# Kernel optimization log

Measured on AMD Instinct MI355X. Metric: run time of the kernel, lower is better.

## Reference

```python
import jax, jax.numpy as jnp
import numpy as np

NUM_CHUNKS = 8
HEAD_DIM = 128
PROJ = 1024       # projection_size (q)
KV_PROJ = 1024    # kv_projection_size
NEG_INF = -1e30


def _rotate_half(x):
    x1, x2 = jnp.split(x, 2, axis=-1)
    return jnp.concatenate((-x2, x1), axis=-1)


def _apply_rope(x, cos, sin):
    # x: [B, S, H, D]; cos/sin: [B, S, 1, rot_dim] with rot_dim == D here
    return x * cos + _rotate_half(x) * sin


def setup_inputs() -> dict:
    key = jax.random.key(0)
    k1, k2, k3 = jax.random.split(key, 3)
    S, B, H = 8192, 1, 1024
    layernorm_output = jax.random.normal(k1, (S, B, H), dtype=jnp.float32)
    # rotary tables, stored [S, 1, 1, rot_dim] (seq-first, like the torch module)
    inv_freq = 1.0 / (10000.0 ** (jnp.arange(0, HEAD_DIM, 2, dtype=jnp.float32) / HEAD_DIM))
    t = jnp.arange(S, dtype=jnp.float32)
    freqs = jnp.einsum('s,d->sd', t, inv_freq)
    emb = jnp.concatenate((freqs, freqs), axis=-1)  # [S, rot_dim]
    freqs_cos = jnp.cos(emb)[:, None, None, :]
    freqs_sin = jnp.sin(emb)[:, None, None, :]
    qkv_weight = jax.random.normal(k2, (PROJ + 2 * KV_PROJ, H), dtype=jnp.float32) * (H ** -0.5)
    qkv_bias = jax.random.normal(k3, (PROJ + 2 * KV_PROJ,), dtype=jnp.float32) * 0.02
    return {
        'layernorm_output': layernorm_output,
        'freqs_cos': freqs_cos,
        'freqs_sin': freqs_sin,
        'qkv_weight': qkv_weight,
        'qkv_bias': qkv_bias,
    }


def reference(layernorm_output, freqs_cos, freqs_sin, qkv_weight, qkv_bias):
    S, B, H = layernorm_output.shape
    cs = S // NUM_CHUNKS  # chunk size
    scale = HEAD_DIM ** -0.5
    # permute(1,0,2,3): [S,1,1,rot] -> [1,S,1,rot] matching [B, seq, head, dim]
    cos = jnp.transpose(freqs_cos, (1, 0, 2, 3))
    sin = jnp.transpose(freqs_sin, (1, 0, 2, 3))

    outs = []
    k_list, v_list = [], []
    for i in range(NUM_CHUNKS):
        st, ed = i * cs, (i + 1) * cs
        x = layernorm_output[st:ed]                      # [cs, B, H]
        qkv = jnp.einsum('sbh,oh->sbo', x, qkv_weight) + qkv_bias
        def to_bshd(t):
            return jnp.transpose(t.reshape(cs, B, -1, HEAD_DIM), (1, 0, 2, 3))
        q = to_bshd(qkv[..., :PROJ])                     # [B, cs, nH, D]
        k = to_bshd(qkv[..., PROJ:PROJ + KV_PROJ])
        v = to_bshd(qkv[..., PROJ + KV_PROJ:])
        cos_i, sin_i = cos[:, st:ed], sin[:, st:ed]
        q = _apply_rope(q, cos_i, sin_i)
        k = _apply_rope(k, cos_i, sin_i)
        k_list.append(k)
        v_list.append(v)

        K = jnp.concatenate(k_list, axis=1)              # [B, (i+1)*cs, nH, D]
        V = jnp.concatenate(v_list, axis=1)
        scores = jnp.einsum('bqhd,bkhd->bhqk', q, K) * scale
        # causal: query global idx st+r attends keys <= st+r; earlier chunks fully visible
        qidx = st + jnp.arange(cs)
        kidx = jnp.arange((i + 1) * cs)
        mask = kidx[None, :] <= qidx[:, None]            # [cs, (i+1)*cs]
        scores = jnp.where(mask[None, None], scores, NEG_INF)
        p = jax.nn.softmax(scores, axis=-1)
        outs.append(jnp.einsum('bhqk,bkhd->bqhd', p, V))
    return jnp.concatenate(outs, axis=1)                 # [B, S, nH, D]
```

## Files before the change

kernel.cpp:

```cpp
#include <hip/hip_runtime.h>
#include <hip/hip_bf16.h>

typedef float f32x4 __attribute__((ext_vector_type(4)));
typedef __bf16 bf16x8 __attribute__((ext_vector_type(8)));
typedef __bf16 bf16x4 __attribute__((ext_vector_type(4)));

#define S_LEN 8192
#define HIDDEN 1024
#define NH 8
#define HD 128

#define QSCALE (0.08838834764831845f * 1.4426950408889634f)
#define FIXMAX 24.0f

__device__ __forceinline__ void async16(const void* g, void* l) {
  __builtin_amdgcn_global_load_lds(
      (const __attribute__((address_space(1))) char*)g,
      (__attribute__((address_space(3))) char*)l, 16, 0, 0);
}

__global__ void cast_bf16_kernel(const float* __restrict__ in, __bf16* __restrict__ out) {
  int i = (blockIdx.x * blockDim.x + threadIdx.x) * 4;
  float4 v = *(const float4*)(in + i);
  bf16x4 o;
  o[0] = (__bf16)v.x; o[1] = (__bf16)v.y; o[2] = (__bf16)v.z; o[3] = (__bf16)v.w;
  *(bf16x4*)(out + i) = o;
}

__global__ __launch_bounds__(256) void gemm_qkv(
    const __bf16* __restrict__ A, const __bf16* __restrict__ W,
    const float* __restrict__ bias,
    __bf16* __restrict__ Qb, __bf16* __restrict__ Kb, __bf16* __restrict__ Vt)
{
  __shared__ __bf16 As[128 * 32];
  __shared__ __bf16 Bs[128 * 32];
  const int t = threadIdx.x;
  const int lane = t & 63;
  const int w = t >> 6;
  const int wy = w >> 1, wx = w & 1;
  const int quad = lane >> 4, l15 = lane & 15;
  const int m0 = blockIdx.y * 128;
  const int n0 = blockIdx.x * 128;
  f32x4 acc[4][4] = {};
  for (int kt = 0; kt < HIDDEN; kt += 32) {
#pragma unroll
    for (int j = 0; j < 2; ++j) {
      int idx = j * 256 + t;
      int row = idx >> 2, c8 = (idx & 3) * 8;
      async16(A + (size_t)(m0 + row) * HIDDEN + kt + c8, As + idx * 8);
      async16(W + (size_t)(n0 + row) * HIDDEN + kt + c8, Bs + idx * 8);
    }
    __syncthreads();
    bf16x8 af[4], bfr[4];
#pragma unroll
    for (int i = 0; i < 4; ++i)
      af[i] = *(const bf16x8*)(As + (wy * 64 + i * 16 + l15) * 32 + quad * 8);
#pragma unroll
    for (int i = 0; i < 4; ++i)
      bfr[i] = *(const bf16x8*)(Bs + (wx * 64 + i * 16 + l15) * 32 + quad * 8);
#pragma unroll
    for (int mt = 0; mt < 4; ++mt)
#pragma unroll
      for (int nt = 0; nt < 4; ++nt)
        acc[mt][nt] = __builtin_amdgcn_mfma_f32_16x16x32_bf16(af[mt], bfr[nt], acc[mt][nt], 0, 0, 0);
    __syncthreads();
  }
  float bv[4];
  int cols[4];
#pragma unroll
  for (int nt = 0; nt < 4; ++nt) {
    cols[nt] = n0 + wx * 64 + nt * 16 + l15;
    bv[nt] = bias[cols[nt]];
  }
#pragma unroll
  for (int mt = 0; mt < 4; ++mt) {
    int srow_base = m0 + wy * 64 + mt * 16 + quad * 4;
#pragma unroll
    for (int nt = 0; nt < 4; ++nt) {
      int c = cols[nt];
#pragma unroll
      for (int r = 0; r < 4; ++r) {
        int s = srow_base + r;
        __bf16 b = (__bf16)(acc[mt][nt][r] + bv[nt]);
        if (n0 < 1024) {
          int h = c >> 7, d = c & 127;
          Qb[(size_t)h * S_LEN * HD + (size_t)s * HD + d] = b;
        } else if (n0 < 2048) {
          int c2 = c - 1024; int h = c2 >> 7, d = c2 & 127;
          Kb[(size_t)h * S_LEN * HD + (size_t)s * HD + d] = b;
        } else {
          int c2 = c - 2048; int h = c2 >> 7, d = c2 & 127;
          Vt[(size_t)h * HD * S_LEN + (size_t)d * S_LEN + s] = b;
        }
      }
    }
  }
}

__global__ void rope_kernel(__bf16* __restrict__ Qb, __bf16* __restrict__ Kb,
                            const float* __restrict__ fcos, const float* __restrict__ fsin)
{
  int gid = blockIdx.x * blockDim.x + threadIdx.x;
  int d = gid & 63;
  int h = (gid >> 6) & 7;
  int s = gid >> 9;
  float c1 = fcos[s * 128 + d],      s1 = fsin[s * 128 + d];
  float c2 = fcos[s * 128 + d + 64], s2 = fsin[s * 128 + d + 64];
  size_t base = (size_t)h * S_LEN * HD + (size_t)s * HD + d;
  float q1 = (float)Qb[base], q2 = (float)Qb[base + 64];
  Qb[base]      = (__bf16)((q1 * c1 - q2 * s1) * QSCALE);
  Qb[base + 64] = (__bf16)((q2 * c2 + q1 * s2) * QSCALE);
  float k1 = (float)Kb[base], k2 = (float)Kb[base + 64];
  Kb[base]      = (__bf16)(k1 * c1 - k2 * s1);
  Kb[base + 64] = (__bf16)(k2 * c2 + k1 * s2);
}

__global__ __launch_bounds__(256, 3) void attn_kernel(
    const __bf16* __restrict__ Qb, const __bf16* __restrict__ Kb,
    const __bf16* __restrict__ Vt, float* __restrict__ out,
    __bf16* __restrict__ partO, float* __restrict__ partML)
{
  __shared__ __bf16 Ks[2][32 * 128];
  __shared__ __bf16 Vs[2][64 * 64];
  __shared__ __bf16 Ps[4 * 1024];
  const int t = threadIdx.x;
  const int lane = t & 63, w = t >> 6;
  const int quad = lane >> 4, l15 = lane & 15;
  const int sw = l15 & 7;
  const int sw6 = l15 & 6;

  const int id = blockIdx.x;
  const int k = id / 24, r = id % 24;
  int head, qi, piece, j0, j1;
  bool isPartial;
  if (r < 16) { qi = 63 - k; piece = r >> 3; head = r & 7;
                j0 = piece * (2 * qi + 2); j1 = j0 + (2 * qi + 2); isPartial = true; }
  else        { qi = 31 - k; piece = 0; head = r - 16;
                j0 = 0; j1 = 4 * qi + 4; isPartial = false; }
  const int qs = qi * 128;
  const int jmax_w = 4 * qi + w;
  const __bf16* Qh = Qb + (size_t)head * S_LEN * HD;
  const __bf16* Kh = Kb + (size_t)head * S_LEN * HD;
  const __bf16* Vh = Vt + (size_t)head * HD * S_LEN;

  bf16x8 qf[2][4];
#pragma unroll
  for (int qg = 0; qg < 2; ++qg) {
    int qrow = qs + w * 32 + qg * 16 + l15;
#pragma unroll
    for (int dk = 0; dk < 4; ++dk)
      qf[qg][dk] = *(const bf16x8*)(Qh + (size_t)qrow * HD + dk * 32 + quad * 8);
  }

  f32x4 o[2][8] = {};
  float l_loc[2] = {0.f, 0.f};
  const f32x4 FM = {-FIXMAX, -FIXMAX, -FIXMAX, -FIXMAX};

  auto stageK = [&](int j, int sel) {
    const __bf16* Kp = Kh + (size_t)(j * 32) * HD;
    __bf16* Kd = &Ks[sel][0];
#pragma unroll
    for (int li = 0; li < 2; ++li) {
      int slot = li * 256 + t;
      int kr = slot >> 4, cp = slot & 15;
      async16(Kp + (size_t)kr * HD + (cp ^ (kr & 7)) * 8, Kd + slot * 8);
    }
  };
  auto stageV = [&](int j, int sel) {
    const __bf16* Vp = Vh + j * 32;
    __bf16* Vd = &Vs[sel][0];
#pragma unroll
    for (int li = 0; li < 2; ++li) {
      int c = li * 256 + t;
      int rr = c >> 3, sl = c & 7;
      int slu = sl ^ (rr & 7);
      int d = 2 * rr + (slu >> 2);
      async16(Vp + (size_t)d * S_LEN + (slu & 3) * 8, Vd + c * 8);
    }
  };

  stageK(j0, 0);
  stageV(j0, 0);

  for (int j = j0; j < j1; ++j) {
    __syncthreads();
    const int cur = (j - j0) & 1;
    if (j + 1 < j1) {
      stageK(j + 1, cur ^ 1);
      stageV(j + 1, cur ^ 1);
    }
    if (j > jmax_w) continue;
    const __bf16* Ksb = &Ks[cur][0];
    const __bf16* Vsb = &Vs[cur][0];

    f32x4 sc[2][2];
#pragma unroll
    for (int mtk = 0; mtk < 2; ++mtk) {
      bf16x8 kf = *(const bf16x8*)(Ksb + (mtk * 16 + l15) * 128 + ((quad ^ sw) * 8));
      sc[0][mtk] = __builtin_amdgcn_mfma_f32_16x16x32_bf16(kf, qf[0][0], FM, 0, 0, 0);
      sc[1][mtk] = __builtin_amdgcn_mfma_f32_16x16x32_bf16(kf, qf[1][0], FM, 0, 0, 0);
    }
#pragma unroll
    for (int dk = 1; dk < 4; ++dk)
#pragma unroll
      for (int mtk = 0; mtk < 2; ++mtk) {
        bf16x8 kf = *(const bf16x8*)(Ksb + (mtk * 16 + l15) * 128 + (((dk * 4 + quad) ^ sw) * 8));
        sc[0][mtk] = __builtin_amdgcn_mfma_f32_16x16x32_bf16(kf, qf[0][dk], sc[0][mtk], 0, 0, 0);
        sc[1][mtk] = __builtin_amdgcn_mfma_f32_16x16x32_bf16(kf, qf[1][dk], sc[1][mtk], 0, 0, 0);
      }

    if (j == jmax_w) {
#pragma unroll
      for (int qg = 0; qg < 2; ++qg)
#pragma unroll
        for (int mtk = 0; mtk < 2; ++mtk)
#pragma unroll
          for (int r2 = 0; r2 < 4; ++r2)
            if (mtk * 16 + quad * 4 + r2 > qg * 16 + l15)
              sc[qg][mtk][r2] = -1e30f;
    }

#pragma unroll
    for (int qg = 0; qg < 2; ++qg)
#pragma unroll
      for (int mtk = 0; mtk < 2; ++mtk) {
        bf16x4 pk;
#pragma unroll
        for (int r2 = 0; r2 < 4; ++r2) {
          float p = __builtin_amdgcn_exp2f(sc[qg][mtk][r2]);
          l_loc[qg] += p;
          pk[r2] = (__bf16)p;
        }
        int slot = (mtk * 4 + quad) ^ sw6;
        *(bf16x4*)(Ps + w * 1024 + qg * 512 + l15 * 32 + slot * 4) = pk;
      }

    bf16x8 pf[2];
#pragma unroll
    for (int qg = 0; qg < 2; ++qg)
      pf[qg] = *(const bf16x8*)(Ps + w * 1024 + qg * 512 + l15 * 32 + (((quad * 2) ^ sw6) * 4));

#pragma unroll
    for (int dt = 0; dt < 8; ++dt) {
      int d = dt * 16 + l15;
      int rr = d >> 1;
      int slu = ((d & 1) << 2) | quad;
      bf16x8 vf = *(const bf16x8*)(Vsb + rr * 64 + ((slu ^ (rr & 7)) * 8));
      o[0][dt] = __builtin_amdgcn_mfma_f32_16x16x32_bf16(vf, pf[0], o[0][dt], 0, 0, 0);
      o[1][dt] = __builtin_amdgcn_mfma_f32_16x16x32_bf16(vf, pf[1], o[1][dt], 0, 0, 0);
    }
  }

  float inv[2], lfull[2];
#pragma unroll
  for (int qg = 0; qg < 2; ++qg) {
    float lv = l_loc[qg];
    lv += __shfl_xor(lv, 16);
    lv += __shfl_xor(lv, 32);
    lfull[qg] = lv;
    inv[qg] = 1.0f / lv;
  }
  if (!isPartial) {
#pragma unroll
    for (int qg = 0; qg < 2; ++qg) {
      int s = qs + w * 32 + qg * 16 + l15;
#pragma unroll
      for (int dt = 0; dt < 8; ++dt) {
        f32x4 v;
#pragma unroll
        for (int r2 = 0; r2 < 4; ++r2) v[r2] = o[qg][dt][r2] * inv[qg];
        *(f32x4*)(out + (size_t)s * 1024 + head * 128 + dt * 16 + quad * 4) = v;
      }
    }
  } else {
    int u = (qi - 32) * 16 + piece * 8 + head;
    __bf16* Op = partO + (size_t)u * 128 * 128;
    float* mlp = partML + u * 256;
#pragma unroll
    for (int qg = 0; qg < 2; ++qg) {
      int row = w * 32 + qg * 16 + l15;
#pragma unroll
      for (int dt = 0; dt < 8; ++dt) {
        bf16x4 pk;
#pragma unroll
        for (int r2 = 0; r2 < 4; ++r2) pk[r2] = (__bf16)(o[qg][dt][r2] * inv[qg]);
        *(bf16x4*)(Op + row * 128 + dt * 16 + quad * 4) = pk;
      }
    }
    if (quad == 0) {
#pragma unroll
      for (int qg = 0; qg < 2; ++qg)
        mlp[w * 32 + qg * 16 + l15] = lfull[qg];
    }
  }
}

__global__ __launch_bounds__(256) void merge_kernel(
    const __bf16* __restrict__ partO, const float* __restrict__ partML,
    float* __restrict__ out)
{
  int b = blockIdx.x;
  int qi = 32 + (b >> 3), head = b & 7;
  int u0 = (qi - 32) * 16 + head;
  int u1 = u0 + 8;
  int t = threadIdx.x;
  int q = t >> 1, dh = (t & 1) * 64;
  float l0 = partML[u0 * 256 + q];
  float l1 = partML[u1 * 256 + q];
  float inv = 1.0f / (l0 + l1);
  float w0 = l0 * inv, w1 = l1 * inv;
  const __bf16* O0 = partO + ((size_t)u0 * 128 + q) * 128 + dh;
  const __bf16* O1 = partO + ((size_t)u1 * 128 + q) * 128 + dh;
  float* op = out + (size_t)(qi * 128 + q) * 1024 + head * 128 + dh;
#pragma unroll
  for (int d = 0; d < 64; d += 8) {
    bf16x8 a = *(const bf16x8*)(O0 + d);
    bf16x8 c = *(const bf16x8*)(O1 + d);
    float4 r0, r1;
    r0.x = w0 * (float)a[0] + w1 * (float)c[0];
    r0.y = w0 * (float)a[1] + w1 * (float)c[1];
    r0.z = w0 * (float)a[2] + w1 * (float)c[2];
    r0.w = w0 * (float)a[3] + w1 * (float)c[3];
    r1.x = w0 * (float)a[4] + w1 * (float)c[4];
    r1.y = w0 * (float)a[5] + w1 * (float)c[5];
    r1.z = w0 * (float)a[6] + w1 * (float)c[6];
    r1.w = w0 * (float)a[7] + w1 * (float)c[7];
    *(float4*)(op + d) = r0;
    *(float4*)(op + d + 4) = r1;
  }
}

extern "C" void kernel_launch(void* const* d_in, const int* in_sizes, int n_in,
                              void* d_out, int out_size, void* d_ws, size_t ws_size,
                              hipStream_t stream)
{
  const float* x    = (const float*)d_in[0];
  const float* fcos = (const float*)d_in[1];
  const float* fsin = (const float*)d_in[2];
  const float* wq   = (const float*)d_in[3];
  const float* bias = (const float*)d_in[4];
  float* out = (float*)d_out;

  char* ws = (char*)d_ws;
  __bf16* xb = (__bf16*)ws;
  __bf16* wb = (__bf16*)(ws + 16777216);
  __bf16* Qb = (__bf16*)(ws + 23068672);
  __bf16* Kb = (__bf16*)(ws + 39845888);
  __bf16* Vt = (__bf16*)(ws + 56623104);

  __bf16* partO = xb;
  float* partML = (float*)wb;

  cast_bf16_kernel<<<8192, 256, 0, stream>>>(x, xb);
  cast_bf16_kernel<<<3072, 256, 0, stream>>>(wq, wb);
  dim3 gg(24, 64);
  gemm_qkv<<<gg, 256, 0, stream>>>(xb, wb, bias, Qb, Kb, Vt);
  rope_kernel<<<16384, 256, 0, stream>>>(Qb, Kb, fcos, fsin);
  attn_kernel<<<768, 256, 0, stream>>>(Qb, Kb, Vt, out, partO, partML);
  merge_kernel<<<256, 256, 0, stream>>>(partO, partML, out);
}
```

Measured before the change: 384.2 us.

## Balance causal attention with stream-K work splitting and atomic accumulation

Replaces the fixed partial/full block split with a stream-K style schedule. Each of 96 blocks per head takes an equal contiguous range of key tiles across the triangular causal work, crossing query-tile boundaries as needed. Unnormalized outputs and row sums are accumulated with float atomics into a zeroed output and a row-sum buffer, and a separate norm kernel divides at the end. This aims to remove load imbalance and the bf16 partial/merge path, at the cost of many scalar atomics, an extra zeroing pass and an extra normalization pass over the output.

```diff
diff --git a/kernel.cpp b/kernel.cpp
--- a/kernel.cpp
+++ b/kernel.cpp
@@ -17,6 +17,10 @@
   __builtin_amdgcn_global_load_lds(
       (const __attribute__((address_space(1))) char*)g,
       (__attribute__((address_space(3))) char*)l, 16, 0, 0);
+}
+
+__device__ __forceinline__ void atomAddF(float* p, float v) {
+  __hip_atomic_fetch_add(p, v, __ATOMIC_RELAXED, __HIP_MEMORY_SCOPE_AGENT);
 }
 
 __global__ void cast_bf16_kernel(const float* __restrict__ in, __bf16* __restrict__ out) {
@@ -25,6 +29,15 @@
   bf16x4 o;
   o[0] = (__bf16)v.x; o[1] = (__bf16)v.y; o[2] = (__bf16)v.z; o[3] = (__bf16)v.w;
   *(bf16x4*)(out + i) = o;
+}
+
+__global__ __launch_bounds__(256) void zero_kernel(float* __restrict__ out,
+                                                   float* __restrict__ Lbuf)
+{
+  size_t i = ((size_t)blockIdx.x * 256 + threadIdx.x) * 4;
+  const f32x4 z = {0.f, 0.f, 0.f, 0.f};
+  if (i < (size_t)S_LEN * 1024) *(f32x4*)(out + i) = z;
+  else                          *(f32x4*)(Lbuf + (i - (size_t)S_LEN * 1024)) = z;
 }
 
 __global__ __launch_bounds__(256) void gemm_qkv(
@@ -118,7 +131,7 @@
 __global__ __launch_bounds__(256, 3) void attn_kernel(
     const __bf16* __restrict__ Qb, const __bf16* __restrict__ Kb,
     const __bf16* __restrict__ Vt, float* __restrict__ out,
-    __bf16* __restrict__ partO, float* __restrict__ partML)
+    float* __restrict__ Lbuf)
 {
   __shared__ __bf16 Ks[2][32 * 128];
   __shared__ __bf16 Vs[2][64 * 64];
@@ -129,31 +142,16 @@
   const int sw = l15 & 7;
   const int sw6 = l15 & 6;
 
-  const int id = blockIdx.x;
-  const int k = id / 24, r = id % 24;
-  int head, qi, piece, j0, j1;
-  bool isPartial;
-  if (r < 16) { qi = 63 - k; piece = r >> 3; head = r & 7;
-                j0 = piece * (2 * qi + 2); j1 = j0 + (2 * qi + 2); isPartial = true; }
-  else        { qi = 31 - k; piece = 0; head = r - 16;
-                j0 = 0; j1 = 4 * qi + 4; isPartial = false; }
-  const int qs = qi * 128;
-  const int jmax_w = 4 * qi + w;
+  const int head = blockIdx.x & 7;
+  const int u = blockIdx.x >> 3;
+  int G = (260 * u) / 3;
+  const int Gend = (260 * (u + 1)) / 3;
+
   const __bf16* Qh = Qb + (size_t)head * S_LEN * HD;
   const __bf16* Kh = Kb + (size_t)head * S_LEN * HD;
   const __bf16* Vh = Vt + (size_t)head * HD * S_LEN;
-
-  bf16x8 qf[2][4];
-#pragma unroll
-  for (int qg = 0; qg < 2; ++qg) {
-    int qrow = qs + w * 32 + qg * 16 + l15;
-#pragma unroll
-    for (int dk = 0; dk < 4; ++dk)
-      qf[qg][dk] = *(const bf16x8*)(Qh + (size_t)qrow * HD + dk * 32 + quad * 8);
-  }
-
-  f32x4 o[2][8] = {};
-  float l_loc[2] = {0.f, 0.f};
+  float* Lh = Lbuf + (size_t)head * S_LEN;
+
   const f32x4 FM = {-FIXMAX, -FIXMAX, -FIXMAX, -FIXMAX};
 
   auto stageK = [&](int j, int sel) {
@@ -179,155 +177,141 @@
     }
   };
 
-  stageK(j0, 0);
-  stageV(j0, 0);
-
-  for (int j = j0; j < j1; ++j) {
+  while (G < Gend) {
+    int qi = (int)((__builtin_sqrtf(2.0f * (float)G + 1.0f) - 1.0f) * 0.5f);
+    while (2 * (qi + 1) * (qi + 2) <= G) ++qi;
+    while (qi > 0 && 2 * qi * (qi + 1) > G) --qi;
+    const int j0 = G - 2 * qi * (qi + 1);
+    const int T = 4 * qi + 4;
+    const int rem = Gend - G;
+    const int j1 = (j0 + rem < T) ? (j0 + rem) : T;
+    G += j1 - j0;
+
+    const int qs = qi * 128;
+    const int jmax_w = 4 * qi + w;
+
+    bf16x8 qf[2][4];
+#pragma unroll
+    for (int qg = 0; qg < 2; ++qg) {
+      int qrow = qs + w * 32 + qg * 16 + l15;
+#pragma unroll
+      for (int dk = 0; dk < 4; ++dk)
+        qf[qg][dk] = *(const bf16x8*)(Qh + (size_t)qrow * HD + dk * 32 + quad * 8);
+    }
+
+    f32x4 o[2][8] = {};
+    float l_loc[2] = {0.f, 0.f};
+
     __syncthreads();
-    const int cur = (j - j0) & 1;
-    if (j + 1 < j1) {
-      stageK(j + 1, cur ^ 1);
-      stageV(j + 1, cur ^ 1);
-    }
-    if (j > jmax_w) continue;
-    const __bf16* Ksb = &Ks[cur][0];
-    const __bf16* Vsb = &Vs[cur][0];
-
-    f32x4 sc[2][2];
-#pragma unroll
-    for (int mtk = 0; mtk < 2; ++mtk) {
-      bf16x8 kf = *(const bf16x8*)(Ksb + (mtk * 16 + l15) * 128 + ((quad ^ sw) * 8));
-      sc[0][mtk] = __builtin_amdgcn_mfma_f32_16x16x32_bf16(kf, qf[0][0], FM, 0, 0, 0);
-      sc[1][mtk] = __builtin_amdgcn_mfma_f32_16x16x32_bf16(kf, qf[1][0], FM, 0, 0, 0);
-    }
-#pragma unroll
-    for (int dk = 1; dk < 4; ++dk)
+    stageK(j0, 0);
+    stageV(j0, 0);
+
+    for (int j = j0; j < j1; ++j) {
+      __syncthreads();
+      const int cur = (j - j0) & 1;
+      if (j + 1 < j1) {
+        stageK(j + 1, cur ^ 1);
+        stageV(j + 1, cur ^ 1);
+      }
+      if (j > jmax_w) continue;
+      const __bf16* Ksb = &Ks[cur][0];
+      const __bf16* Vsb = &Vs[cur][0];
+
+      f32x4 sc[2][2];
 #pragma unroll
       for (int mtk = 0; mtk < 2; ++mtk) {
-        bf16x8 kf = *(const bf16x8*)(Ksb + (mtk * 16 + l15) * 128 + (((dk * 4 + quad) ^ sw) * 8));
-        sc[0][mtk] = __builtin_amdgcn_mfma_f32_16x16x32_bf16(kf, qf[0][dk], sc[0][mtk], 0, 0, 0);
-        sc[1][mtk] = __builtin_amdgcn_mfma_f32_16x16x32_bf16(kf, qf[1][dk], sc[1][mtk], 0, 0, 0);
-      }
-
-    if (j == jmax_w) {
+        bf16x8 kf = *(const bf16x8*)(Ksb + (mtk * 16 + l15) * 128 + ((quad ^ sw) * 8));
+        sc[0][mtk] = __builtin_amdgcn_mfma_f32_16x16x32_bf16(kf, qf[0][0], FM, 0, 0, 0);
+        sc[1][mtk] = __builtin_amdgcn_mfma_f32_16x16x32_bf16(kf, qf[1][0], FM, 0, 0, 0);
+      }
+#pragma unroll
+      for (int dk = 1; dk < 4; ++dk)
+#pragma unroll
+        for (int mtk = 0; mtk < 2; ++mtk) {
+          bf16x8 kf = *(const bf16x8*)(Ksb + (mtk * 16 + l15) * 128 + (((dk * 4 + quad) ^ sw) * 8));
+          sc[0][mtk] = __builtin_amdgcn_mfma_f32_16x16x32_bf16(kf, qf[0][dk], sc[0][mtk], 0, 0, 0);
+          sc[1][mtk] = __builtin_amdgcn_mfma_f32_16x16x32_bf16(kf, qf[1][dk], sc[1][mtk], 0, 0, 0);
+        }
+
+      if (j == jmax_w) {
+#pragma unroll
+        for (int qg = 0; qg < 2; ++qg)
+#pragma unroll
+          for (int mtk = 0; mtk < 2; ++mtk)
+#pragma unroll
+            for (int r2 = 0; r2 < 4; ++r2)
+              if (mtk * 16 + quad * 4 + r2 > qg * 16 + l15)
+                sc[qg][mtk][r2] = -1e30f;
+      }
+
 #pragma unroll
       for (int qg = 0; qg < 2; ++qg)
 #pragma unroll
-        for (int mtk = 0; mtk < 2; ++mtk)
-#pragma unroll
-          for (int r2 = 0; r2 < 4; ++r2)
-            if (mtk * 16 + quad * 4 + r2 > qg * 16 + l15)
-              sc[qg][mtk][r2] = -1e30f;
-    }
-
-#pragma unroll
-    for (int qg = 0; qg < 2; ++qg)
-#pragma unroll
-      for (int mtk = 0; mtk < 2; ++mtk) {
-        bf16x4 pk;
-#pragma unroll
-        for (int r2 = 0; r2 < 4; ++r2) {
-          float p = __builtin_amdgcn_exp2f(sc[qg][mtk][r2]);
-          l_loc[qg] += p;
-          pk[r2] = (__bf16)p;
+        for (int mtk = 0; mtk < 2; ++mtk) {
+          bf16x4 pk;
+#pragma unroll
+          for (int r2 = 0; r2 < 4; ++r2) {
+            float p = __builtin_amdgcn_exp2f(sc[qg][mtk][r2]);
+            l_loc[qg] += p;
+            pk[r2] = (__bf16)p;
+          }
+          int slot = (mtk * 4 + quad) ^ sw6;
+          *(bf16x4*)(Ps + w * 1024 + qg * 512 + l15 * 32 + slot * 4) = pk;
         }
-        int slot = (mtk * 4 + quad) ^ sw6;
-        *(bf16x4*)(Ps + w * 1024 + qg * 512 + l15 * 32 + slot * 4) = pk;
-      }
-
-    bf16x8 pf[2];
-#pragma unroll
-    for (int qg = 0; qg < 2; ++qg)
-      pf[qg] = *(const bf16x8*)(Ps + w * 1024 + qg * 512 + l15 * 32 + (((quad * 2) ^ sw6) * 4));
-
-#pragma unroll
-    for (int dt = 0; dt < 8; ++dt) {
-      int d = dt * 16 + l15;
-      int rr = d >> 1;
-      int slu = ((d & 1) << 2) | quad;
-      bf16x8 vf = *(const bf16x8*)(Vsb + rr * 64 + ((slu ^ (rr & 7)) * 8));
-      o[0][dt] = __builtin_amdgcn_mfma_f32_16x16x32_bf16(vf, pf[0], o[0][dt], 0, 0, 0);
-      o[1][dt] = __builtin_amdgcn_mfma_f32_16x16x32_bf16(vf, pf[1], o[1][dt], 0, 0, 0);
-    }
-  }
-
-  float inv[2], lfull[2];
-#pragma unroll
-  for (int qg = 0; qg < 2; ++qg) {
-    float lv = l_loc[qg];
-    lv += __shfl_xor(lv, 16);
-    lv += __shfl_xor(lv, 32);
-    lfull[qg] = lv;
-    inv[qg] = 1.0f / lv;
-  }
-  if (!isPartial) {
+
+      bf16x8 pf[2];
+#pragma unroll
+      for (int qg = 0; qg < 2; ++qg)
+        pf[qg] = *(const bf16x8*)(Ps + w * 1024 + qg * 512 + l15 * 32 + (((quad * 2) ^ sw6) * 4));
+
+#pragma unroll
+      for (int dt = 0; dt < 8; ++dt) {
+        int d = dt * 16 + l15;
+        int rr = d >> 1;
+        int slu = ((d & 1) << 2) | quad;
+        bf16x8 vf = *(const bf16x8*)(Vsb + rr * 64 + ((slu ^ (rr & 7)) * 8));
+        o[0][dt] = __builtin_amdgcn_mfma_f32_16x16x32_bf16(vf, pf[0], o[0][dt], 0, 0, 0);
+        o[1][dt] = __builtin_amdgcn_mfma_f32_16x16x32_bf16(vf, pf[1], o[1][dt], 0, 0, 0);
+      }
+    }
+
+    float lfull[2];
+#pragma unroll
+    for (int qg = 0; qg < 2; ++qg) {
+      float lv = l_loc[qg];
+      lv += __shfl_xor(lv, 16);
+      lv += __shfl_xor(lv, 32);
+      lfull[qg] = lv;
+    }
 #pragma unroll
     for (int qg = 0; qg < 2; ++qg) {
       int s = qs + w * 32 + qg * 16 + l15;
-#pragma unroll
-      for (int dt = 0; dt < 8; ++dt) {
-        f32x4 v;
-#pragma unroll
-        for (int r2 = 0; r2 < 4; ++r2) v[r2] = o[qg][dt][r2] * inv[qg];
-        *(f32x4*)(out + (size_t)s * 1024 + head * 128 + dt * 16 + quad * 4) = v;
-      }
-    }
-  } else {
-    int u = (qi - 32) * 16 + piece * 8 + head;
-    __bf16* Op = partO + (size_t)u * 128 * 128;
-    float* mlp = partML + u * 256;
-#pragma unroll
-    for (int qg = 0; qg < 2; ++qg) {
-      int row = w * 32 + qg * 16 + l15;
-#pragma unroll
-      for (int dt = 0; dt < 8; ++dt) {
-        bf16x4 pk;
-#pragma unroll
-        for (int r2 = 0; r2 < 4; ++r2) pk[r2] = (__bf16)(o[qg][dt][r2] * inv[qg]);
-        *(bf16x4*)(Op + row * 128 + dt * 16 + quad * 4) = pk;
-      }
+      float* op = out + (size_t)s * 1024 + head * 128 + quad * 4;
+#pragma unroll
+      for (int dt = 0; dt < 8; ++dt)
+#pragma unroll
+        for (int r2 = 0; r2 < 4; ++r2)
+          atomAddF(op + dt * 16 + r2, o[qg][dt][r2]);
     }
     if (quad == 0) {
 #pragma unroll
       for (int qg = 0; qg < 2; ++qg)
-        mlp[w * 32 + qg * 16 + l15] = lfull[qg];
+        atomAddF(Lh + qs + w * 32 + qg * 16 + l15, lfull[qg]);
     }
   }
 }
 
-__global__ __launch_bounds__(256) void merge_kernel(
-    const __bf16* __restrict__ partO, const float* __restrict__ partML,
-    float* __restrict__ out)
-{
-  int b = blockIdx.x;
-  int qi = 32 + (b >> 3), head = b & 7;
-  int u0 = (qi - 32) * 16 + head;
-  int u1 = u0 + 8;
-  int t = threadIdx.x;
-  int q = t >> 1, dh = (t & 1) * 64;
-  float l0 = partML[u0 * 256 + q];
-  float l1 = partML[u1 * 256 + q];
-  float inv = 1.0f / (l0 + l1);
-  float w0 = l0 * inv, w1 = l1 * inv;
-  const __bf16* O0 = partO + ((size_t)u0 * 128 + q) * 128 + dh;
-  const __bf16* O1 = partO + ((size_t)u1 * 128 + q) * 128 + dh;
-  float* op = out + (size_t)(qi * 128 + q) * 1024 + head * 128 + dh;
-#pragma unroll
-  for (int d = 0; d < 64; d += 8) {
-    bf16x8 a = *(const bf16x8*)(O0 + d);
-    bf16x8 c = *(const bf16x8*)(O1 + d);
-    float4 r0, r1;
-    r0.x = w0 * (float)a[0] + w1 * (float)c[0];
-    r0.y = w0 * (float)a[1] + w1 * (float)c[1];
-    r0.z = w0 * (float)a[2] + w1 * (float)c[2];
-    r0.w = w0 * (float)a[3] + w1 * (float)c[3];
-    r1.x = w0 * (float)a[4] + w1 * (float)c[4];
-    r1.y = w0 * (float)a[5] + w1 * (float)c[5];
-    r1.z = w0 * (float)a[6] + w1 * (float)c[6];
-    r1.w = w0 * (float)a[7] + w1 * (float)c[7];
-    *(float4*)(op + d) = r0;
-    *(float4*)(op + d + 4) = r1;
-  }
+__global__ __launch_bounds__(256) void norm_kernel(float* __restrict__ out,
+                                                   const float* __restrict__ L)
+{
+  int s = blockIdx.x;
+  int col = threadIdx.x * 4;
+  int h = col >> 7;
+  float inv = 1.0f / L[(size_t)h * S_LEN + s];
+  float* p = out + (size_t)s * 1024 + col;
+  f32x4 v = *(const f32x4*)p;
+  v[0] *= inv; v[1] *= inv; v[2] *= inv; v[3] *= inv;
+  *(f32x4*)p = v;
 }
 
 extern "C" void kernel_launch(void* const* d_in, const int* in_sizes, int n_in,
@@ -348,14 +332,14 @@
   __bf16* Kb = (__bf16*)(ws + 39845888);
   __bf16* Vt = (__bf16*)(ws + 56623104);
 
-  __bf16* partO = xb;
-  float* partML = (float*)wb;
+  float* Lbuf = (float*)ws;
 
   cast_bf16_kernel<<<8192, 256, 0, stream>>>(x, xb);
   cast_bf16_kernel<<<3072, 256, 0, stream>>>(wq, wb);
   dim3 gg(24, 64);
   gemm_qkv<<<gg, 256, 0, stream>>>(xb, wb, bias, Qb, Kb, Vt);
   rope_kernel<<<16384, 256, 0, stream>>>(Qb, Kb, fcos, fsin);
-  attn_kernel<<<768, 256, 0, stream>>>(Qb, Kb, Vt, out, partO, partML);
-  merge_kernel<<<256, 256, 0, stream>>>(partO, partML, out);
-}
+  zero_kernel<<<8256, 256, 0, stream>>>(out, Lbuf);
+  attn_kernel<<<768, 256, 0, stream>>>(Qb, Kb, Vt, out, Lbuf);
+  norm_kernel<<<8192, 256, 0, stream>>>(out, Lbuf);
+}
```

Result: slower. 551.3 us (+43.5%).
